# Kernel tuning notes

Hardware: AMD Instinct MI355X
Metric: run time of the kernel (lower is better)

## Reference

```python
import jax, jax.numpy as jnp
import numpy as np

N = 50000; E = 600000; D = 128; NB = 20; L = 3; H = 64; NG = 512; ZMAX = 100
CUTOFF = 5.0

def setup_inputs() -> dict:
    key = jax.random.key(0)
    ks = jax.random.split(key, 32)
    inp = {}
    inp['at_no'] = jax.random.randint(ks[0], (N,), 0, ZMAX)
    inp['pos'] = jax.random.normal(ks[1], (N, 3), dtype=jnp.float32) * 3.0
    inp['edge_index'] = jax.random.randint(ks[2], (2, E), 0, N)
    inp['batch'] = jnp.sort(jax.random.randint(ks[3], (N,), 0, NG))
    def w(k, shape, fan_in):
        return (jax.random.normal(k, shape, dtype=jnp.float32) / np.sqrt(fan_in)).astype(jnp.float32)
    inp['emb'] = w(ks[4], (ZMAX, D), 1.0)
    # per-block filter net: rbf -> 3D
    inp['Wf'] = w(ks[5], (L, NB, 3 * D), NB); inp['bf'] = jnp.zeros((L, 3 * D), jnp.float32)
    # per-block message scalar MLP: D -> D -> 3D
    inp['Wm1'] = w(ks[6], (L, D, D), D);      inp['bm1'] = jnp.zeros((L, D), jnp.float32)
    inp['Wm2'] = w(ks[7], (L, D, 3 * D), D);  inp['bm2'] = jnp.zeros((L, 3 * D), jnp.float32)
    # per-block update: U, V channel-mixing on vectors; MLP 2D -> D -> 3D
    inp['U'] = w(ks[8], (L, D, D), D)
    inp['V'] = w(ks[9], (L, D, D), D)
    inp['Wu1'] = w(ks[10], (L, 2 * D, D), 2 * D); inp['bu1'] = jnp.zeros((L, D), jnp.float32)
    inp['Wu2'] = w(ks[11], (L, D, 3 * D), D);     inp['bu2'] = jnp.zeros((L, 3 * D), jnp.float32)
    # scalar output head: D -> H -> 1, graph sum
    inp['Wo1'] = w(ks[12], (D, H), D); inp['bo1'] = jnp.zeros((H,), jnp.float32)
    inp['Wo2'] = w(ks[13], (H, 1), H); inp['bo2'] = jnp.zeros((1,), jnp.float32)
    return inp

def _painn(at_no, pos, edge_index, batch, emb, Wf, bf, Wm1, bm1, Wm2, bm2,
           U, V, Wu1, bu1, Wu2, bu2, Wo1, bo1, Wo2, bo2):
    src, dst = edge_index[0], edge_index[1]
    vec = pos[dst] - pos[src]                       # [E,3]
    dist = jnp.sqrt(jnp.sum(vec * vec, axis=-1, keepdims=True) + 1e-12)  # [E,1]
    dirv = vec / dist                               # [E,3] (rsh l=1)
    n = jnp.arange(1, NB + 1, dtype=jnp.float32)
    rbf = jnp.sin(n * jnp.pi * dist / CUTOFF) / dist            # [E,NB] Bessel
    fcut = 0.5 * (jnp.cos(jnp.pi * dist / CUTOFF) + 1.0) * (dist < CUTOFF)  # [E,1]

    x = emb[at_no]                                  # [N,D]
    v = jnp.zeros((x.shape[0], 3, D), x.dtype)      # [N,3,D]

    for l in range(L):
        # ---- message ----
        filt = (rbf @ Wf[l] + bf[l]) * fcut                     # [E,3D]
        phi = jax.nn.silu(x @ Wm1[l] + bm1[l]) @ Wm2[l] + bm2[l]  # [N,3D]
        m = phi[src] * filt                                     # [E,3D]
        ds, dv1, dv2 = m[:, :D], m[:, D:2 * D], m[:, 2 * D:]
        dv = dv1[:, None, :] * dirv[:, :, None] + dv2[:, None, :] * v[src]  # [E,3,D]
        x = x + jax.ops.segment_sum(ds, dst, num_segments=N)
        v = v + jax.ops.segment_sum(dv, dst, num_segments=N)
        # ---- update ----
        Uv = jnp.einsum('ncd,de->nce', v, U[l])
        Vv = jnp.einsum('ncd,de->nce', v, V[l])
        Vn = jnp.sqrt(jnp.sum(Vv * Vv, axis=1) + 1e-8)          # [N,D]
        a = jax.nn.silu(jnp.concatenate([x, Vn], axis=-1) @ Wu1[l] + bu1[l]) @ Wu2[l] + bu2[l]
        avv, asv, ass = a[:, :D], a[:, D:2 * D], a[:, 2 * D:]
        x = x + ass + asv * jnp.sum(Uv * Vv, axis=1)
        v = v + avv[:, None, :] * Uv

    node_out = jax.nn.silu(x @ Wo1 + bo1) @ Wo2 + bo2           # [N,1]
    return jax.ops.segment_sum(node_out, batch, num_segments=NG)  # [NG,1]

def reference(at_no, pos, edge_index, batch, emb, Wf, bf, Wm1, bm1, Wm2, bm2,
              U, V, Wu1, bu1, Wu2, bu2, Wo1, bo1, Wo2, bo2):
    return _painn(at_no, pos, edge_index, batch, emb, Wf, bf, Wm1, bm1, Wm2, bm2,
                  U, V, Wu1, bu1, Wu2, bu2, Wo1, bo1, Wo2, bo2)
```

## Files before the change

### kernel.cpp

```cpp
#include <hip/hip_runtime.h>
#include <math.h>

#define NN 50000
#define NE 600000
#define ECAP 230000
#define DD 128
#define D3 384
#define NB_ 20
#define HH 64
#define NG_ 512
#define LSZ 180224

typedef short v8s __attribute__((ext_vector_type(8)));
typedef short v4sh __attribute__((ext_vector_type(4)));
typedef float v4f __attribute__((ext_vector_type(4)));

__device__ __forceinline__ float silu_f(float z) { return z / (1.0f + expf(-z)); }

__device__ __forceinline__ short f2bf(float f) {
  unsigned u = __float_as_uint(f);
  u += 0x7FFF + ((u >> 16) & 1);
  return (short)(u >> 16);
}
__device__ __forceinline__ float bf2f(short s) {
  return __uint_as_float(((unsigned)(unsigned short)s) << 16);
}
__device__ __forceinline__ void split2(float x, short& h, short& l) {
  h = f2bf(x);
  l = f2bf(x - bf2f(h));
}
__device__ __forceinline__ void split_store4(float4 f, short* hp, short* lp) {
  short h0,l0,h1,l1,h2,l2,h3,l3;
  split2(f.x,h0,l0); split2(f.y,h1,l1); split2(f.z,h2,l2); split2(f.w,h3,l3);
  v4sh hv = {h0,h1,h2,h3}, lv = {l0,l1,l2,l3};
  *(v4sh*)hp = hv; *(v4sh*)lp = lv;
}
#define MFMA3(acc, ah, al, bh, bl) \
  acc = __builtin_amdgcn_mfma_f32_16x16x32_bf16(ah, bh, acc, 0, 0, 0); \
  acc = __builtin_amdgcn_mfma_f32_16x16x32_bf16(al, bh, acc, 0, 0, 0); \
  acc = __builtin_amdgcn_mfma_f32_16x16x32_bf16(ah, bl, acc, 0, 0, 0);

__global__ void zero_f_kernel(float* __restrict__ p, long n) {
  long i = (long)blockIdx.x * blockDim.x + threadIdx.x;
  long s = (long)gridDim.x * blockDim.x;
  for (; i < n; i += s) p[i] = 0.0f;
}

__global__ void zero_i_kernel(int* __restrict__ p, long n) {
  long i = (long)blockIdx.x * blockDim.x + threadIdx.x;
  long s = (long)gridDim.x * blockDim.x;
  for (; i < n; i += s) p[i] = 0;
}

__global__ void init_x_kernel(const int* __restrict__ at_no, const float* __restrict__ emb,
                              float* __restrict__ x) {
  int i = blockIdx.x * blockDim.x + threadIdx.x;
  if (i >= NN * DD) return;
  x[i] = emb[at_no[i >> 7] * DD + (i & 127)];
}

__global__ void prep_w_kernel(const float* __restrict__ Wm1, const float* __restrict__ Wm2,
                              const float* __restrict__ U, const float* __restrict__ V,
                              const float* __restrict__ Wu1, const float* __restrict__ Wu2,
                              short* __restrict__ hi, short* __restrict__ lo) {
  int idx = blockIdx.x * 256 + threadIdx.x;
  if (idx >= 3 * LSZ) return;
  int l = idx / LSZ, r = idx % LSZ;
  const float* src; int K, N, nk;
  if (r < 16384)       { src = Wm1 + (size_t)l*16384; K = 128; N = 128; nk = r; }
  else if (r < 65536)  { src = Wm2 + (size_t)l*49152; K = 128; N = 384; nk = r - 16384; }
  else if (r < 81920)  { src = U   + (size_t)l*16384; K = 128; N = 128; nk = r - 65536; }
  else if (r < 98304)  { src = V   + (size_t)l*16384; K = 128; N = 128; nk = r - 81920; }
  else if (r < 131072) { src = Wu1 + (size_t)l*32768; K = 256; N = 128; nk = r - 98304; }
  else                 { src = Wu2 + (size_t)l*49152; K = 128; N = 384; nk = r - 131072; }
  int n = nk / K, k = nk - n * K;
  float xx = src[(size_t)k * N + n];
  short h = f2bf(xx);
  hi[idx] = h;
  lo[idx] = f2bf(xx - bf2f(h));
}

__global__ void hist_kernel(const int* __restrict__ ei, const float* __restrict__ pos,
                            int* __restrict__ counts) {
  int e = blockIdx.x * blockDim.x + threadIdx.x;
  if (e >= NE) return;
  int s = ei[e], d = ei[NE + e];
  float dx = pos[3*d]   - pos[3*s];
  float dy = pos[3*d+1] - pos[3*s+1];
  float dz = pos[3*d+2] - pos[3*s+2];
  float d2 = dx*dx + dy*dy + dz*dz + 1e-12f;
  if (d2 < 25.0f) atomicAdd(&counts[d], 1);
}

__global__ void scan_kernel(const int* __restrict__ counts, int* __restrict__ indptr, int n) {
  __shared__ int sm[1024];
  __shared__ int carry_s;
  if (threadIdx.x == 0) carry_s = 0;
  __syncthreads();
  for (int start = 0; start < n; start += 1024) {
    int i = start + (int)threadIdx.x;
    int val = (i < n) ? counts[i] : 0;
    sm[threadIdx.x] = val;
    __syncthreads();
    for (int off = 1; off < 1024; off <<= 1) {
      int t = (threadIdx.x >= (unsigned)off) ? sm[threadIdx.x - off] : 0;
      __syncthreads();
      sm[threadIdx.x] += t;
      __syncthreads();
    }
    int c = carry_s;
    if (i < n) indptr[i] = c + sm[threadIdx.x] - val;
    __syncthreads();
    if (threadIdx.x == 0) carry_s = c + sm[1023];
    __syncthreads();
  }
  if (threadIdx.x == 0) indptr[n] = carry_s;
}

__global__ void fill_kernel(const int* __restrict__ ei, const float* __restrict__ pos,
                            const int* __restrict__ indptr, int* __restrict__ cursor,
                            int* __restrict__ srcs, float4* __restrict__ eg1,
                            float4* __restrict__ eg2) {
  int e = blockIdx.x * blockDim.x + threadIdx.x;
  if (e >= NE) return;
  int s = ei[e], d = ei[NE + e];
  float dx = pos[3*d]   - pos[3*s];
  float dy = pos[3*d+1] - pos[3*s+1];
  float dz = pos[3*d+2] - pos[3*s+2];
  float d2 = dx*dx + dy*dy + dz*dz + 1e-12f;
  if (d2 < 25.0f) {
    int p = atomicAdd(&cursor[d], 1);
    int slot = indptr[d] + p;
    float dist = sqrtf(d2);
    float inv = 1.0f / dist;
    float wang = 0.62831853071795864769f * dist;
    float s1 = __sinf(wang), c1 = __cosf(wang);
    float fc = 0.5f * (c1 + 1.0f);
    srcs[slot] = s;
    eg1[slot] = make_float4(s1, c1, fc, fc * inv);
    eg2[slot] = make_float4(dx * inv, dy * inv, dz * inv, 0.0f);
  }
}

template<bool SILU>
__global__ void __launch_bounds__(256) mfma_gemm_kernel(
    const float* A, const short* __restrict__ Bth, const short* __restrict__ Btl,
    const float* __restrict__ bias, float* C, int M) {
  __shared__ short As2[2 * 32 * 136];
  #define ASH(r,c) As2[(r)*136 + (c)]
  #define ASL(r,c) As2[4352 + (r)*136 + (c)]
  int tid = threadIdx.x;
  long r0 = (long)blockIdx.x * 32;
  #pragma unroll
  for (int i = 0; i < 4; i++) {
    int lin = i*256 + tid;
    int r = lin >> 5, c4 = lin & 31;
    long row = r0 + r; if (row >= M) row = M - 1;
    float4 f = *(const float4*)(A + row*128 + c4*4);
    split_store4(f, &ASH(r, c4*4), &ASL(r, c4*4));
  }
  __syncthreads();
  int lane = tid & 63, wv = tid >> 6;
  int l15 = lane & 15, q = lane >> 4;
  v4f acc[2][2] = {};
  #pragma unroll
  for (int s = 0; s < 4; s++) {
    v8s ah[2], al[2];
    #pragma unroll
    for (int mt = 0; mt < 2; mt++) {
      ah[mt] = *(const v8s*)&ASH(mt*16 + l15, s*32 + q*8);
      al[mt] = *(const v8s*)&ASL(mt*16 + l15, s*32 + q*8);
    }
    #pragma unroll
    for (int nt = 0; nt < 2; nt++) {
      int n = (2*wv + nt)*16 + l15;
      v8s bh = *(const v8s*)(Bth + (long)n*128 + s*32 + q*8);
      v8s bl = *(const v8s*)(Btl + (long)n*128 + s*32 + q*8);
      #pragma unroll
      for (int mt = 0; mt < 2; mt++) { MFMA3(acc[mt][nt], ah[mt], al[mt], bh, bl); }
    }
  }
  #pragma unroll
  for (int nt = 0; nt < 2; nt++) {
    int n = (2*wv + nt)*16 + l15;
    float bb = bias[n];
    #pragma unroll
    for (int mt = 0; mt < 2; mt++)
      #pragma unroll
      for (int i = 0; i < 4; i++) {
        long row = r0 + mt*16 + q*4 + i;
        if (row < M) {
          float val = acc[mt][nt][i] + bb;
          if constexpr (SILU) val = silu_f(val);
          C[row*128 + n] = val;
        }
      }
  }
  #undef ASH
  #undef ASL
}

__global__ void __launch_bounds__(512) mfma_gemm_phi_kernel(
    const float* A, const short* __restrict__ Bth, const short* __restrict__ Btl,
    const float* __restrict__ bias,
    float* __restrict__ C0, float* __restrict__ C1, float* C2, int M) {
  __shared__ short As2[2 * 32 * 136];
  #define ASH(r,c) As2[(r)*136 + (c)]
  #define ASL(r,c) As2[4352 + (r)*136 + (c)]
  int tid = threadIdx.x;
  long r0 = (long)blockIdx.x * 32;
  #pragma unroll
  for (int i = 0; i < 2; i++) {
    int lin = i*512 + tid;
    int r = lin >> 5, c4 = lin & 31;
    long row = r0 + r; if (row >= M) row = M - 1;
    float4 f = *(const float4*)(A + row*128 + c4*4);
    split_store4(f, &ASH(r, c4*4), &ASL(r, c4*4));
  }
  __syncthreads();
  int lane = tid & 63, wv = tid >> 6;
  int l15 = lane & 15, q = lane >> 4;
  v4f acc[2][3] = {};
  #pragma unroll
  for (int s = 0; s < 4; s++) {
    v8s ah[2], al[2];
    #pragma unroll
    for (int mt = 0; mt < 2; mt++) {
      ah[mt] = *(const v8s*)&ASH(mt*16 + l15, s*32 + q*8);
      al[mt] = *(const v8s*)&ASL(mt*16 + l15, s*32 + q*8);
    }
    #pragma unroll
    for (int j = 0; j < 3; j++) {
      int n = (wv*3 + j)*16 + l15;
      v8s bh = *(const v8s*)(Bth + (long)n*128 + s*32 + q*8);
      v8s bl = *(const v8s*)(Btl + (long)n*128 + s*32 + q*8);
      #pragma unroll
      for (int mt = 0; mt < 2; mt++) { MFMA3(acc[mt][j], ah[mt], al[mt], bh, bl); }
    }
  }
  #pragma unroll
  for (int j = 0; j < 3; j++) {
    int n = (wv*3 + j)*16 + l15;
    int sl = n >> 7, col = n & 127;
    float* C = (sl == 0) ? C0 : (sl == 1) ? C1 : C2;
    float bb = bias[n];
    #pragma unroll
    for (int mt = 0; mt < 2; mt++)
      #pragma unroll
      for (int i = 0; i < 4; i++) {
        long row = r0 + mt*16 + q*4 + i;
        if (row < M) C[row*128 + col] = acc[mt][j][i] + bb;
      }
  }
  #undef ASH
  #undef ASL
}

__global__ void __launch_bounds__(128) msg012_kernel(
    const float* __restrict__ phi0, const float* __restrict__ phi1,
    const float* __restrict__ phi2, const float* __restrict__ vA,
    float* __restrict__ vB, float* __restrict__ x,
    const int* __restrict__ srcs, const float4* __restrict__ eg1,
    const float4* __restrict__ eg2, const int* __restrict__ indptr,
    const float* __restrict__ Wf_l, const float* __restrict__ bf_l) {
  const long NND = (long)NN*DD;
  int d = threadIdx.x;
  float wf0[NB_], wf1[NB_], wf2[NB_];
  #pragma unroll
  for (int k = 0; k < NB_; k++) {
    wf0[k] = Wf_l[k*D3 + d];
    wf1[k] = Wf_l[k*D3 + DD + d];
    wf2[k] = Wf_l[k*D3 + 2*DD + d];
  }
  float bf0 = bf_l[d], bf1 = bf_l[DD + d], bf2 = bf_l[2*DD + d];
  int n0 = blockIdx.x * 8;
  for (int j = 0; j < 8; j++) {
    int n = n0 + j;
    int t = indptr[n], end = indptr[n+1];
    float xacc = 0.f, a0 = 0.f, a1 = 0.f, a2 = 0.f;
    float4 g1C = {}, g2C = {};
    float p0C = 0.f, p1C = 0.f, p2C = 0.f, w0C = 0.f, w1C = 0.f, w2C = 0.f;
    if (t < end) {
      int s0 = srcs[t]; g1C = eg1[t]; g2C = eg2[t];
      long b = (long)s0*DD + d;
      p0C = phi0[b]; p1C = phi1[b]; p2C = phi2[b];
      w0C = vA[b]; w1C = vA[NND + b]; w2C = vA[2*NND + b];
    }
    for (; t < end; t++) {
      float4 g = g1C, dv = g2C;
      float p0 = p0C, p1 = p1C, p2 = p2C, w0 = w0C, w1 = w1C, w2 = w2C;
      if (t + 1 < end) {
        int sN = srcs[t+1]; g1C = eg1[t+1]; g2C = eg2[t+1];
        long b = (long)sN*DD + d;
        p0C = phi0[b]; p1C = phi1[b]; p2C = phi2[b];
        w0C = vA[b]; w1C = vA[NND + b]; w2C = vA[2*NND + b];
      }
      float c2 = 2.0f * g.y;
      float rkm1 = 0.f, rk = g.x, dot0 = 0.f, dot1 = 0.f, dot2 = 0.f;
      #pragma unroll
      for (int k = 0; k < NB_; k++) {
        dot0 = fmaf(rk, wf0[k], dot0);
        dot1 = fmaf(rk, wf1[k], dot1);
        dot2 = fmaf(rk, wf2[k], dot2);
        float rn = fmaf(c2, rk, -rkm1);
        rkm1 = rk; rk = rn;
      }
      xacc = fmaf(p0, bf0*g.z + g.w*dot0, xacc);
      float m1 = p1 * (bf1*g.z + g.w*dot1);
      float m2 = p2 * (bf2*g.z + g.w*dot2);
      a0 = fmaf(m1, dv.x, fmaf(m2, w0, a0));
      a1 = fmaf(m1, dv.y, fmaf(m2, w1, a1));
      a2 = fmaf(m1, dv.z, fmaf(m2, w2, a2));
    }
    long b = (long)n*DD + d;
    x[b] += xacc;
    vB[b]         = vA[b]         + a0;
    vB[NND + b]   = vA[NND + b]   + a1;
    vB[2*NND + b] = vA[2*NND + b] + a2;
  }
}

__global__ void __launch_bounds__(512) uva_kernel(
    float* __restrict__ x, float* __restrict__ v,
    const short* __restrict__ Uth, const short* __restrict__ Utl,
    const short* __restrict__ Vth, const short* __restrict__ Vtl,
    const short* __restrict__ W1h, const short* __restrict__ W1l, const float* __restrict__ b1,
    const short* __restrict__ W2h, const short* __restrict__ W2l, const float* __restrict__ b2) {
  __shared__ short smem[13824];
  #define VSH(r,c)  smem[(r)*136 + (c)]
  #define VSL(r,c)  smem[6528 + (r)*136 + (c)]
  #define CATH(r,c) smem[(r)*280 + (c)]
  #define CATL(r,c) smem[4480 + (r)*280 + (c)]
  #define T2H(r,c)  smem[8960 + (r)*152 + (c)]
  #define T2L(r,c)  smem[11392 + (r)*152 + (c)]
  const long NND = (long)NN*DD;
  int tid = threadIdx.x;
  long nb = (long)blockIdx.x * 16;
  int lane = tid & 63, wv = tid >> 6;
  int l15 = lane & 15, q = lane >> 4;
  int d = wv*16 + l15;
  float vold[4][3], xold[4];
  #pragma unroll
  for (int i = 0; i < 4; i++) {
    long row = nb + q*4 + i;
    xold[i] = x[row*DD + d];
    #pragma unroll
    for (int c = 0; c < 3; c++) vold[i][c] = v[(long)c*NND + row*DD + d];
  }
  #pragma unroll
  for (int i = 0; i < 3; i++) {
    int lin = i*512 + tid;
    int r = lin >> 5, c4 = lin & 31;
    int c = r >> 4, nr = r & 15;
    float4 f = *(const float4*)(v + (long)c*NND + (nb + nr)*DD + c4*4);
    split_store4(f, &VSH(r, c4*4), &VSL(r, c4*4));
  }
  __syncthreads();
  v4f aU[3] = {}, aV[3] = {};
  #pragma unroll
  for (int s = 0; s < 4; s++) {
    long boff = (long)d*128 + s*32 + q*8;
    v8s buh = *(const v8s*)(Uth + boff);
    v8s bul = *(const v8s*)(Utl + boff);
    v8s bvh = *(const v8s*)(Vth + boff);
    v8s bvl = *(const v8s*)(Vtl + boff);
    #pragma unroll
    for (int c = 0; c < 3; c++) {
      v8s ah = *(const v8s*)&VSH(c*16 + l15, s*32 + q*8);
      v8s al = *(const v8s*)&VSL(c*16 + l15, s*32 + q*8);
      MFMA3(aU[c], ah, al, buh, bul);
      MFMA3(aV[c], ah, al, bvh, bvl);
    }
  }
  float sreg[4], vn2[4];
  #pragma unroll
  for (int i = 0; i < 4; i++) {
    sreg[i] = aU[0][i]*aV[0][i] + aU[1][i]*aV[1][i] + aU[2][i]*aV[2][i];
    vn2[i]  = aV[0][i]*aV[0][i] + aV[1][i]*aV[1][i] + aV[2][i]*aV[2][i];
  }
  __syncthreads();
  {
    int r = tid >> 5, c4 = tid & 31;
    float4 f = *(const float4*)(x + (nb + r)*DD + c4*4);
    split_store4(f, &CATH(r, c4*4), &CATL(r, c4*4));
  }
  #pragma unroll
  for (int i = 0; i < 4; i++) {
    short h, l;
    split2(sqrtf(vn2[i] + 1e-8f), h, l);
    CATH(q*4 + i, 128 + d) = h; CATL(q*4 + i, 128 + d) = l;
  }
  __syncthreads();
  {
    v4f acc = {};
    #pragma unroll
    for (int s = 0; s < 8; s++) {
      v8s ah = *(const v8s*)&CATH(l15, s*32 + q*8);
      v8s al = *(const v8s*)&CATL(l15, s*32 + q*8);
      v8s bh = *(const v8s*)(W1h + (long)d*256 + s*32 + q*8);
      v8s bl = *(const v8s*)(W1l + (long)d*256 + s*32 + q*8);
      MFMA3(acc, ah, al, bh, bl);
    }
    float bb = b1[d];
    #pragma unroll
    for (int i = 0; i < 4; i++) {
      short h, l;
      split2(silu_f(acc[i] + bb), h, l);
      T2H(q*4 + i, d) = h; T2L(q*4 + i, d) = l;
    }
  }
  __syncthreads();
  {
    v4f acc[3] = {};
    #pragma unroll
    for (int s = 0; s < 4; s++) {
      v8s ah = *(const v8s*)&T2H(l15, s*32 + q*8);
      v8s al = *(const v8s*)&T2L(l15, s*32 + q*8);
      #pragma unroll
      for (int g = 0; g < 3; g++) {
        int n = g*128 + d;
        v8s bh = *(const v8s*)(W2h + (long)n*128 + s*32 + q*8);
        v8s bl = *(const v8s*)(W2l + (long)n*128 + s*32 + q*8);
        MFMA3(acc[g], ah, al, bh, bl);
      }
    }
    float bavv = b2[d], basv = b2[128 + d], bass = b2[256 + d];
    #pragma unroll
    for (int i = 0; i < 4; i++) {
      long row = nb + q*4 + i;
      float avv = acc[0][i] + bavv;
      float asv = acc[1][i] + basv;
      float ass = acc[2][i] + bass;
      x[row*DD + d] = xold[i] + ass + asv * sreg[i];
      #pragma unroll
      for (int c = 0; c < 3; c++)
        v[(long)c*NND + row*DD + d] = fmaf(avv, aU[c][i], vold[i][c]);
    }
  }
  #undef VSH
  #undef VSL
  #undef CATH
  #undef CATL
  #undef T2H
  #undef T2L
}

__global__ void __launch_bounds__(256) out_kernel(
    const float* __restrict__ x, const float* __restrict__ Wo1,
    const float* __restrict__ bo1, const float* __restrict__ Wo2,
    const float* __restrict__ bo2, const int* __restrict__ batch,
    float* __restrict__ out) {
  __shared__ float xs[4][132];
  int tid = threadIdx.x;
  long n0 = (long)blockIdx.x * 4;
  if (tid < 128) {
    int r = tid >> 5, c4 = tid & 31;
    *(float4*)&xs[r][c4*4] = *(const float4*)(x + (n0 + r)*128 + c4*4);
  }
  __syncthreads();
  int wv = tid >> 6, t = tid & 63;
  float acc = bo1[t];
  #pragma unroll 16
  for (int k = 0; k < DD; k++) acc = fmaf(xs[wv][k], Wo1[k*HH + t], acc);
  float val = silu_f(acc) * Wo2[t];
  #pragma unroll
  for (int off = 32; off > 0; off >>= 1) val += __shfl_down(val, off);
  if (t == 0) atomicAdd(&out[batch[n0 + wv]], val + bo2[0]);
}

extern "C" void kernel_launch(void* const* d_in, const int* in_sizes, int n_in,
                              void* d_out, int out_size, void* d_ws, size_t ws_size,
                              hipStream_t stream) {
  const int*   at_no = (const int*)d_in[0];
  const float* pos   = (const float*)d_in[1];
  const int*   ei    = (const int*)d_in[2];
  const int*   batch = (const int*)d_in[3];
  const float* emb   = (const float*)d_in[4];
  const float* Wf    = (const float*)d_in[5];
  const float* bfp   = (const float*)d_in[6];
  const float* Wm1   = (const float*)d_in[7];
  const float* bm1   = (const float*)d_in[8];
  const float* Wm2   = (const float*)d_in[9];
  const float* bm2   = (const float*)d_in[10];
  const float* U     = (const float*)d_in[11];
  const float* V     = (const float*)d_in[12];
  const float* Wu1   = (const float*)d_in[13];
  const float* bu1   = (const float*)d_in[14];
  const float* Wu2   = (const float*)d_in[15];
  const float* bu2   = (const float*)d_in[16];
  const float* Wo1   = (const float*)d_in[17];
  const float* bo1   = (const float*)d_in[18];
  const float* Wo2   = (const float*)d_in[19];
  const float* bo2   = (const float*)d_in[20];
  float* out = (float*)d_out;

  char* w = (char*)d_ws;
  auto alloc = [&](size_t bytes) -> void* {
    void* p = (void*)w;
    w += (bytes + 255) & ~(size_t)255;
    return p;
  };
  float*  x      = (float*)alloc(sizeof(float)*(size_t)NN*DD);
  float*  v_a    = (float*)alloc(sizeof(float)*(size_t)NN*D3);
  float*  v_b    = (float*)alloc(sizeof(float)*(size_t)NN*D3);
  float*  t1     = (float*)alloc(sizeof(float)*(size_t)NN*DD);
  float*  phiS   = (float*)alloc(sizeof(float)*(size_t)NN*DD);
  float*  phi0   = (float*)alloc(sizeof(float)*(size_t)NN*DD);
  short*  wbh    = (short*)alloc(sizeof(short)*(size_t)3*LSZ);
  short*  wbl    = (short*)alloc(sizeof(short)*(size_t)3*LSZ);
  int*    srcs   = (int*)alloc(sizeof(int)*(size_t)ECAP);
  float4* eg1    = (float4*)alloc(sizeof(float4)*(size_t)ECAP);
  float4* eg2    = (float4*)alloc(sizeof(float4)*(size_t)ECAP);
  int*    indptr = (int*)alloc(sizeof(int)*((size_t)NN+1));
  int*    counts = (int*)alloc(sizeof(int)*(size_t)NN);

  if ((size_t)(w - (char*)d_ws) > ws_size) {
    zero_f_kernel<<<2, 256, 0, stream>>>(out, NG_);
    return;
  }

  zero_f_kernel<<<2048, 256, 0, stream>>>(v_a, (long)NN*D3);
  zero_f_kernel<<<2, 256, 0, stream>>>(out, NG_);
  zero_i_kernel<<<64, 256, 0, stream>>>(counts, NN);
  init_x_kernel<<<(NN*DD + 255)/256, 256, 0, stream>>>(at_no, emb, x);
  prep_w_kernel<<<(3*LSZ + 255)/256, 256, 0, stream>>>(Wm1, Wm2, U, V, Wu1, Wu2, wbh, wbl);
  hist_kernel<<<(NE + 255)/256, 256, 0, stream>>>(ei, pos, counts);
  scan_kernel<<<1, 1024, 0, stream>>>(counts, indptr, NN);
  zero_i_kernel<<<64, 256, 0, stream>>>(counts, NN);
  fill_kernel<<<(NE + 255)/256, 256, 0, stream>>>(ei, pos, indptr, counts, srcs, eg1, eg2);

  const int MB = (NN + 31) / 32;
  float* vcur = v_a;
  float* vnext = v_b;
  for (int l = 0; l < 3; l++) {
    const float* Wf_l  = Wf  + (size_t)l*NB_*D3;
    const float* bf_l  = bfp + (size_t)l*D3;
    const float* bm1_l = bm1 + (size_t)l*DD;
    const float* bm2_l = bm2 + (size_t)l*D3;
    const float* bu1_l = bu1 + (size_t)l*DD;
    const float* bu2_l = bu2 + (size_t)l*D3;
    const short* Lh = wbh + (size_t)l*LSZ;
    const short* Ll = wbl + (size_t)l*LSZ;
    const short* Wm1h = Lh,          *Wm1L = Ll;
    const short* Wm2h = Lh + 16384,  *Wm2L = Ll + 16384;
    const short* Uh   = Lh + 65536,  *UL   = Ll + 65536;
    const short* Vh   = Lh + 81920,  *VL   = Ll + 81920;
    const short* Wu1h = Lh + 98304,  *Wu1L = Ll + 98304;
    const short* Wu2h = Lh + 131072, *Wu2L = Ll + 131072;

    mfma_gemm_kernel<true><<<MB, 256, 0, stream>>>(x, Wm1h, Wm1L, bm1_l, t1, NN);
    mfma_gemm_phi_kernel<<<MB, 512, 0, stream>>>(t1, Wm2h, Wm2L, bm2_l, phi0, phiS, t1, NN);
    msg012_kernel<<<NN/8, 128, 0, stream>>>(phi0, phiS, t1, vcur, vnext, x,
                                            srcs, eg1, eg2, indptr, Wf_l, bf_l);
    uva_kernel<<<NN/16, 512, 0, stream>>>(x, vnext, Uh, UL, Vh, VL,
                                          Wu1h, Wu1L, bu1_l, Wu2h, Wu2L, bu2_l);

    float* tmp = vcur; vcur = vnext; vnext = tmp;
  }

  out_kernel<<<NN/4, 256, 0, stream>>>(x, Wo1, bo1, Wo2, bo2, batch, out);

  (void)in_sizes; (void)n_in; (void)out_size; (void)ws_size;
}
```

Baseline: 1.496 ms.

## Fuse message aggregation and update kernels, keeping node state in shared memory

Merges the per-node message gather kernel into the update kernel. Each 512-thread block first aggregates messages for its 16 nodes into fp32 shared memory, then runs the U/V and MLP MFMA stages on that data. This avoids writing and re-reading x and v through global memory between the two kernels. The bf16 hi/lo split now happens at MFMA operand load time rather than when staging, which adds conversion work per operand read. The message phase now runs with 4 groups of 128 threads sharing one block with the MFMA phase, which changes occupancy and can let imbalanced edge loads stall the whole block.

```diff
diff --git a/kernel.cpp b/kernel.cpp
--- a/kernel.cpp
+++ b/kernel.cpp
@@ -29,6 +29,11 @@
   h = f2bf(x);
   l = f2bf(x - bf2f(h));
 }
+#define SPLIT8(f0, f1, ah, al) { short h,l; \
+  split2(f0.x,h,l); ah[0]=h; al[0]=l;  split2(f0.y,h,l); ah[1]=h; al[1]=l; \
+  split2(f0.z,h,l); ah[2]=h; al[2]=l;  split2(f0.w,h,l); ah[3]=h; al[3]=l; \
+  split2(f1.x,h,l); ah[4]=h; al[4]=l;  split2(f1.y,h,l); ah[5]=h; al[5]=l; \
+  split2(f1.z,h,l); ah[6]=h; al[6]=l;  split2(f1.w,h,l); ah[7]=h; al[7]=l; }
 __device__ __forceinline__ void split_store4(float4 f, short* hp, short* lp) {
   short h0,l0,h1,l1,h2,l2,h3,l3;
   split2(f.x,h0,l0); split2(f.y,h1,l1); split2(f.z,h2,l2); split2(f.w,h3,l3);
@@ -256,106 +261,85 @@
   #undef ASL
 }
 
-__global__ void __launch_bounds__(128) msg012_kernel(
+__global__ void __launch_bounds__(512) muva_kernel(
     const float* __restrict__ phi0, const float* __restrict__ phi1,
     const float* __restrict__ phi2, const float* __restrict__ vA,
     float* __restrict__ vB, float* __restrict__ x,
     const int* __restrict__ srcs, const float4* __restrict__ eg1,
     const float4* __restrict__ eg2, const int* __restrict__ indptr,
-    const float* __restrict__ Wf_l, const float* __restrict__ bf_l) {
-  const long NND = (long)NN*DD;
-  int d = threadIdx.x;
-  float wf0[NB_], wf1[NB_], wf2[NB_];
-  #pragma unroll
-  for (int k = 0; k < NB_; k++) {
-    wf0[k] = Wf_l[k*D3 + d];
-    wf1[k] = Wf_l[k*D3 + DD + d];
-    wf2[k] = Wf_l[k*D3 + 2*DD + d];
-  }
-  float bf0 = bf_l[d], bf1 = bf_l[DD + d], bf2 = bf_l[2*DD + d];
-  int n0 = blockIdx.x * 8;
-  for (int j = 0; j < 8; j++) {
-    int n = n0 + j;
-    int t = indptr[n], end = indptr[n+1];
-    float xacc = 0.f, a0 = 0.f, a1 = 0.f, a2 = 0.f;
-    float4 g1C = {}, g2C = {};
-    float p0C = 0.f, p1C = 0.f, p2C = 0.f, w0C = 0.f, w1C = 0.f, w2C = 0.f;
-    if (t < end) {
-      int s0 = srcs[t]; g1C = eg1[t]; g2C = eg2[t];
-      long b = (long)s0*DD + d;
-      p0C = phi0[b]; p1C = phi1[b]; p2C = phi2[b];
-      w0C = vA[b]; w1C = vA[NND + b]; w2C = vA[2*NND + b];
-    }
-    for (; t < end; t++) {
-      float4 g = g1C, dv = g2C;
-      float p0 = p0C, p1 = p1C, p2 = p2C, w0 = w0C, w1 = w1C, w2 = w2C;
-      if (t + 1 < end) {
-        int sN = srcs[t+1]; g1C = eg1[t+1]; g2C = eg2[t+1];
-        long b = (long)sN*DD + d;
-        p0C = phi0[b]; p1C = phi1[b]; p2C = phi2[b];
-        w0C = vA[b]; w1C = vA[NND + b]; w2C = vA[2*NND + b];
-      }
-      float c2 = 2.0f * g.y;
-      float rkm1 = 0.f, rk = g.x, dot0 = 0.f, dot1 = 0.f, dot2 = 0.f;
-      #pragma unroll
-      for (int k = 0; k < NB_; k++) {
-        dot0 = fmaf(rk, wf0[k], dot0);
-        dot1 = fmaf(rk, wf1[k], dot1);
-        dot2 = fmaf(rk, wf2[k], dot2);
-        float rn = fmaf(c2, rk, -rkm1);
-        rkm1 = rk; rk = rn;
-      }
-      xacc = fmaf(p0, bf0*g.z + g.w*dot0, xacc);
-      float m1 = p1 * (bf1*g.z + g.w*dot1);
-      float m2 = p2 * (bf2*g.z + g.w*dot2);
-      a0 = fmaf(m1, dv.x, fmaf(m2, w0, a0));
-      a1 = fmaf(m1, dv.y, fmaf(m2, w1, a1));
-      a2 = fmaf(m1, dv.z, fmaf(m2, w2, a2));
-    }
-    long b = (long)n*DD + d;
-    x[b] += xacc;
-    vB[b]         = vA[b]         + a0;
-    vB[NND + b]   = vA[NND + b]   + a1;
-    vB[2*NND + b] = vA[2*NND + b] + a2;
-  }
-}
-
-__global__ void __launch_bounds__(512) uva_kernel(
-    float* __restrict__ x, float* __restrict__ v,
+    const float* __restrict__ Wf_l, const float* __restrict__ bf_l,
     const short* __restrict__ Uth, const short* __restrict__ Utl,
     const short* __restrict__ Vth, const short* __restrict__ Vtl,
     const short* __restrict__ W1h, const short* __restrict__ W1l, const float* __restrict__ b1,
     const short* __restrict__ W2h, const short* __restrict__ W2l, const float* __restrict__ b2) {
-  __shared__ short smem[13824];
-  #define VSH(r,c)  smem[(r)*136 + (c)]
-  #define VSL(r,c)  smem[6528 + (r)*136 + (c)]
-  #define CATH(r,c) smem[(r)*280 + (c)]
-  #define CATL(r,c) smem[4480 + (r)*280 + (c)]
-  #define T2H(r,c)  smem[8960 + (r)*152 + (c)]
-  #define T2L(r,c)  smem[11392 + (r)*152 + (c)]
+  __shared__ float smem[8704];
+  #define VN(r,c)  smem[(r)*136 + (c)]
+  #define XN(r,c)  smem[6528 + (r)*136 + (c)]
+  #define CAT(r,c) smem[(r)*272 + (c)]
+  #define T2(r,c)  smem[4352 + (r)*136 + (c)]
   const long NND = (long)NN*DD;
   int tid = threadIdx.x;
   long nb = (long)blockIdx.x * 16;
+  {
+    int g = tid >> 7, d = tid & 127;
+    float wf0[NB_], wf1[NB_], wf2[NB_];
+    #pragma unroll
+    for (int k = 0; k < NB_; k++) {
+      wf0[k] = Wf_l[k*D3 + d];
+      wf1[k] = Wf_l[k*D3 + DD + d];
+      wf2[k] = Wf_l[k*D3 + 2*DD + d];
+    }
+    float bf0 = bf_l[d], bf1 = bf_l[DD + d], bf2 = bf_l[2*DD + d];
+    for (int j = 0; j < 4; j++) {
+      int nr = 4*g + j;
+      long n = nb + nr;
+      int t = indptr[n], end = indptr[n+1];
+      float xacc = 0.f, a0 = 0.f, a1 = 0.f, a2 = 0.f;
+      float4 g1C = {}, g2C = {};
+      float p0C = 0.f, p1C = 0.f, p2C = 0.f, w0C = 0.f, w1C = 0.f, w2C = 0.f;
+      if (t < end) {
+        int s0 = srcs[t]; g1C = eg1[t]; g2C = eg2[t];
+        long b = (long)s0*DD + d;
+        p0C = phi0[b]; p1C = phi1[b]; p2C = phi2[b];
+        w0C = vA[b]; w1C = vA[NND + b]; w2C = vA[2*NND + b];
+      }
+      for (; t < end; t++) {
+        float4 gg = g1C, dv = g2C;
+        float p0 = p0C, p1 = p1C, p2 = p2C, w0 = w0C, w1 = w1C, w2 = w2C;
+        if (t + 1 < end) {
+          int sN = srcs[t+1]; g1C = eg1[t+1]; g2C = eg2[t+1];
+          long b = (long)sN*DD + d;
+          p0C = phi0[b]; p1C = phi1[b]; p2C = phi2[b];
+          w0C = vA[b]; w1C = vA[NND + b]; w2C = vA[2*NND + b];
+        }
+        float c2 = 2.0f * gg.y;
+        float rkm1 = 0.f, rk = gg.x, dot0 = 0.f, dot1 = 0.f, dot2 = 0.f;
+        #pragma unroll
+        for (int k = 0; k < NB_; k++) {
+          dot0 = fmaf(rk, wf0[k], dot0);
+          dot1 = fmaf(rk, wf1[k], dot1);
+          dot2 = fmaf(rk, wf2[k], dot2);
+          float rn = fmaf(c2, rk, -rkm1);
+          rkm1 = rk; rk = rn;
+        }
+        xacc = fmaf(p0, bf0*gg.z + gg.w*dot0, xacc);
+        float m1 = p1 * (bf1*gg.z + gg.w*dot1);
+        float m2 = p2 * (bf2*gg.z + gg.w*dot2);
+        a0 = fmaf(m1, dv.x, fmaf(m2, w0, a0));
+        a1 = fmaf(m1, dv.y, fmaf(m2, w1, a1));
+        a2 = fmaf(m1, dv.z, fmaf(m2, w2, a2));
+      }
+      long b = n*DD + d;
+      XN(nr, d) = x[b] + xacc;
+      VN(nr, d)      = vA[b]         + a0;
+      VN(16 + nr, d) = vA[NND + b]   + a1;
+      VN(32 + nr, d) = vA[2*NND + b] + a2;
+    }
+  }
+  __syncthreads();
   int lane = tid & 63, wv = tid >> 6;
   int l15 = lane & 15, q = lane >> 4;
   int d = wv*16 + l15;
-  float vold[4][3], xold[4];
-  #pragma unroll
-  for (int i = 0; i < 4; i++) {
-    long row = nb + q*4 + i;
-    xold[i] = x[row*DD + d];
-    #pragma unroll
-    for (int c = 0; c < 3; c++) vold[i][c] = v[(long)c*NND + row*DD + d];
-  }
-  #pragma unroll
-  for (int i = 0; i < 3; i++) {
-    int lin = i*512 + tid;
-    int r = lin >> 5, c4 = lin & 31;
-    int c = r >> 4, nr = r & 15;
-    float4 f = *(const float4*)(v + (long)c*NND + (nb + nr)*DD + c4*4);
-    split_store4(f, &VSH(r, c4*4), &VSL(r, c4*4));
-  }
-  __syncthreads();
   v4f aU[3] = {}, aV[3] = {};
   #pragma unroll
   for (int s = 0; s < 4; s++) {
@@ -366,8 +350,10 @@
     v8s bvl = *(const v8s*)(Vtl + boff);
     #pragma unroll
     for (int c = 0; c < 3; c++) {
-      v8s ah = *(const v8s*)&VSH(c*16 + l15, s*32 + q*8);
-      v8s al = *(const v8s*)&VSL(c*16 + l15, s*32 + q*8);
+      float4 f0 = *(const float4*)&VN(c*16 + l15, s*32 + q*8);
+      float4 f1 = *(const float4*)&VN(c*16 + l15, s*32 + q*8 + 4);
+      v8s ah, al;
+      SPLIT8(f0, f1, ah, al);
       MFMA3(aU[c], ah, al, buh, bul);
       MFMA3(aV[c], ah, al, bvh, bvl);
     }
@@ -378,44 +364,46 @@
     sreg[i] = aU[0][i]*aV[0][i] + aU[1][i]*aV[1][i] + aU[2][i]*aV[2][i];
     vn2[i]  = aV[0][i]*aV[0][i] + aV[1][i]*aV[1][i] + aV[2][i]*aV[2][i];
   }
+  float vold[4][3];
+  #pragma unroll
+  for (int i = 0; i < 4; i++)
+    #pragma unroll
+    for (int c = 0; c < 3; c++) vold[i][c] = VN(c*16 + q*4 + i, d);
   __syncthreads();
   {
     int r = tid >> 5, c4 = tid & 31;
-    float4 f = *(const float4*)(x + (nb + r)*DD + c4*4);
-    split_store4(f, &CATH(r, c4*4), &CATL(r, c4*4));
-  }
-  #pragma unroll
-  for (int i = 0; i < 4; i++) {
-    short h, l;
-    split2(sqrtf(vn2[i] + 1e-8f), h, l);
-    CATH(q*4 + i, 128 + d) = h; CATL(q*4 + i, 128 + d) = l;
-  }
+    *(float4*)&CAT(r, c4*4) = *(const float4*)&XN(r, c4*4);
+  }
+  #pragma unroll
+  for (int i = 0; i < 4; i++)
+    CAT(q*4 + i, 128 + d) = sqrtf(vn2[i] + 1e-8f);
   __syncthreads();
   {
     v4f acc = {};
     #pragma unroll
     for (int s = 0; s < 8; s++) {
-      v8s ah = *(const v8s*)&CATH(l15, s*32 + q*8);
-      v8s al = *(const v8s*)&CATL(l15, s*32 + q*8);
+      float4 f0 = *(const float4*)&CAT(l15, s*32 + q*8);
+      float4 f1 = *(const float4*)&CAT(l15, s*32 + q*8 + 4);
+      v8s ah, al;
+      SPLIT8(f0, f1, ah, al);
       v8s bh = *(const v8s*)(W1h + (long)d*256 + s*32 + q*8);
       v8s bl = *(const v8s*)(W1l + (long)d*256 + s*32 + q*8);
       MFMA3(acc, ah, al, bh, bl);
     }
     float bb = b1[d];
     #pragma unroll
-    for (int i = 0; i < 4; i++) {
-      short h, l;
-      split2(silu_f(acc[i] + bb), h, l);
-      T2H(q*4 + i, d) = h; T2L(q*4 + i, d) = l;
-    }
+    for (int i = 0; i < 4; i++)
+      T2(q*4 + i, d) = silu_f(acc[i] + bb);
   }
   __syncthreads();
   {
     v4f acc[3] = {};
     #pragma unroll
     for (int s = 0; s < 4; s++) {
-      v8s ah = *(const v8s*)&T2H(l15, s*32 + q*8);
-      v8s al = *(const v8s*)&T2L(l15, s*32 + q*8);
+      float4 f0 = *(const float4*)&T2(l15, s*32 + q*8);
+      float4 f1 = *(const float4*)&T2(l15, s*32 + q*8 + 4);
+      v8s ah, al;
+      SPLIT8(f0, f1, ah, al);
       #pragma unroll
       for (int g = 0; g < 3; g++) {
         int n = g*128 + d;
@@ -427,22 +415,21 @@
     float bavv = b2[d], basv = b2[128 + d], bass = b2[256 + d];
     #pragma unroll
     for (int i = 0; i < 4; i++) {
-      long row = nb + q*4 + i;
+      int lr = q*4 + i;
+      long row = nb + lr;
       float avv = acc[0][i] + bavv;
       float asv = acc[1][i] + basv;
       float ass = acc[2][i] + bass;
-      x[row*DD + d] = xold[i] + ass + asv * sreg[i];
+      x[row*DD + d] = CAT(lr, d) + ass + asv * sreg[i];
       #pragma unroll
       for (int c = 0; c < 3; c++)
-        v[(long)c*NND + row*DD + d] = fmaf(avv, aU[c][i], vold[i][c]);
-    }
-  }
-  #undef VSH
-  #undef VSL
-  #undef CATH
-  #undef CATL
-  #undef T2H
-  #undef T2L
+        vB[(long)c*NND + row*DD + d] = fmaf(avv, aU[c][i], vold[i][c]);
+    }
+  }
+  #undef VN
+  #undef XN
+  #undef CAT
+  #undef T2
 }
 
 __global__ void __launch_bounds__(256) out_kernel(
@@ -550,10 +537,10 @@
 
     mfma_gemm_kernel<true><<<MB, 256, 0, stream>>>(x, Wm1h, Wm1L, bm1_l, t1, NN);
     mfma_gemm_phi_kernel<<<MB, 512, 0, stream>>>(t1, Wm2h, Wm2L, bm2_l, phi0, phiS, t1, NN);
-    msg012_kernel<<<NN/8, 128, 0, stream>>>(phi0, phiS, t1, vcur, vnext, x,
-                                            srcs, eg1, eg2, indptr, Wf_l, bf_l);
-    uva_kernel<<<NN/16, 512, 0, stream>>>(x, vnext, Uh, UL, Vh, VL,
-                                          Wu1h, Wu1L, bu1_l, Wu2h, Wu2L, bu2_l);
+    muva_kernel<<<NN/16, 512, 0, stream>>>(phi0, phiS, t1, vcur, vnext, x,
+                                           srcs, eg1, eg2, indptr, Wf_l, bf_l,
+                                           Uh, UL, Vh, VL,
+                                           Wu1h, Wu1L, bu1_l, Wu2h, Wu2L, bu2_l);
 
     float* tmp = vcur; vcur = vnext; vnext = tmp;
   }
```

New measurement: 1.477 ms. About the same (-1.3%).
